# Optimization experiments

Hardware: AMD Instinct MI355X
Metric: run time of the kernel (lower is better)

The kernel has to match this reference:

```python
import jax, jax.numpy as jnp
import numpy as np

B, S, D_IN, D = 2, 192, 1024, 128  # batch, seq_len, input_dim, triaffine_dim


def setup_inputs() -> dict:
    key = jax.random.key(0)
    ks = jax.random.split(key, 10)
    g = lambda k, sh, sc: jax.random.normal(k, sh, jnp.float32) * sc
    return {
        "x": g(ks[0], (B, S, D_IN), 1.0),
        "Wp": g(ks[1], (D_IN, D), 0.02), "bp": jnp.zeros((D,), jnp.float32),
        "Wh": g(ks[2], (D_IN, D), 0.02), "bh": jnp.zeros((D,), jnp.float32),
        "Wt": g(ks[3], (D_IN, D), 0.02), "bt": jnp.zeros((D,), jnp.float32),
        "W_span_ph": g(ks[4], (D, D, D), 0.02),
        "W_span_pt": g(ks[5], (D, D, D), 0.02),
        "W_ph_sib": g(ks[6], (D, D, D), 0.02),
        "W_pt_sib": g(ks[7], (D, D, D), 0.02),
        "W_ph_cop": g(ks[8], (D, D, D), 0.02),
        "W_pt_cop": g(ks[9], (D, D, D), 0.02),
    }


def _mlp(x, W, b):
    # supar-style MLP: Linear + LeakyReLU(0.1); dropout is identity at eval time
    return jax.nn.leaky_relu(x @ W + b, negative_slope=0.1)


def _triaffine(x, y, z, w):
    # supar Triaffine (n_out=1, no bias): s[b,z,x,y] = x_i W_ikj z_k y_j
    wz = jnp.einsum('bzk,ikj->bzij', z, w)          # [b,s,d,d]
    return jnp.einsum('bxi,bzij,byj->bzxy', x, wz, y)  # [b,s,s,s]


def _sym(s):
    # s.triu() + s.triu(1).transpose(-1,-2) over last two dims
    n = s.shape[-1]
    up = jnp.triu(jnp.ones((n, n), bool))
    up1 = jnp.triu(jnp.ones((n, n), bool), 1)
    zero = jnp.zeros((), s.dtype)
    return jnp.where(up, s, zero) + jnp.swapaxes(jnp.where(up1, s, zero), -1, -2)


def reference(x, Wp, bp, Wh, bh, Wt, bt,
              W_span_ph, W_span_pt, W_ph_sib, W_pt_sib, W_ph_cop, W_pt_cop):
    p = _mlp(x, Wp, bp)
    sh = _mlp(x, Wh, bh)   # shared_span: sh_mlp = h_mlp
    st = _mlp(x, Wt, bt)   # shared_span: st_mlp = t_mlp
    span_pst = _sym(_triaffine(sh, st, p, W_span_pt))
    span_psh = _sym(_triaffine(sh, st, p, W_span_ph))
    ph_sib = _sym(_triaffine(sh, sh, p, W_ph_sib))
    pt_sib = _sym(_triaffine(st, st, p, W_pt_sib))
    # co-parent scores: [b,z,x,y] -> permute(0,2,3,1) -> [b,x,y,z]
    ph_cop = jnp.transpose(_triaffine(p, p, sh, W_ph_cop), (0, 2, 3, 1))
    pt_cop = jnp.transpose(_sym(_triaffine(p, p, st, W_pt_cop)), (0, 2, 3, 1))
    return (span_psh, span_pst, ph_sib, pt_sib, ph_cop, pt_cop)
```

## Files before the change

kernel.cpp:

```cpp
#include <hip/hip_runtime.h>

#define SS 192
#define DD 128
#define SAN 16384
#define PITCH 136

typedef short bf8v __attribute__((ext_vector_type(8)));
typedef float f4v  __attribute__((ext_vector_type(4)));

__device__ __forceinline__ unsigned short f2bf(float f) {
    union { float f; unsigned u; } v; v.f = f;
    unsigned r = v.u + 0x7fffu + ((v.u >> 16) & 1u);
    return (unsigned short)(r >> 16);
}

__device__ __forceinline__ f4v mfma16(bf8v a, bf8v b, f4v c) {
    return __builtin_amdgcn_mfma_f32_16x16x32_bf16(a, b, c, 0, 0, 0);
}

__global__ __launch_bounds__(256) void proj_kernel(
    const float* __restrict__ x,
    const float* __restrict__ Wp, const float* __restrict__ bp,
    const float* __restrict__ Wh, const float* __restrict__ bh,
    const float* __restrict__ Wt, const float* __restrict__ bt,
    unsigned short* __restrict__ Pb, unsigned short* __restrict__ SHb,
    unsigned short* __restrict__ STb)
{
    __shared__ float xs[8 * 1024];
    int r0 = blockIdx.x * 8;
    int w  = blockIdx.y;
    const float* W    = (w == 0) ? Wp : (w == 1) ? Wh : Wt;
    const float* bias = (w == 0) ? bp : (w == 1) ? bh : bt;
    unsigned short* O = (w == 0) ? Pb : (w == 1) ? SHb : STb;
    int tid = threadIdx.x;
    for (int u = tid; u < 2048; u += 256)
        *(float4*)(&xs[u * 4]) = *(const float4*)(&x[(size_t)r0 * 1024 + (size_t)u * 4]);
    __syncthreads();
    int col = tid & 127, rg = tid >> 7;
    float acc[4] = {0.f, 0.f, 0.f, 0.f};
    for (int k = 0; k < 1024; ++k) {
        float wv = W[(size_t)k * 128 + col];
        #pragma unroll
        for (int r = 0; r < 4; ++r) acc[r] += xs[(rg * 4 + r) * 1024 + k] * wv;
    }
    float bb = bias[col];
    #pragma unroll
    for (int r = 0; r < 4; ++r) {
        float v = acc[r] + bb;
        v = v > 0.f ? v : 0.1f * v;
        O[(size_t)(r0 + rg * 4 + r) * 128 + col] = f2bf(v);
    }
}

__global__ __launch_bounds__(256) void prep_rev(
    const float* __restrict__ w0, const float* __restrict__ w1,
    const float* __restrict__ w2, const float* __restrict__ w3,
    unsigned short* __restrict__ Wprep)
{
    __shared__ float tile[32][33];
    int sel = blockIdx.z;
    const float* in = (sel == 0) ? w0 : (sel == 1) ? w1 : (sel == 2) ? w2 : w3;
    unsigned short* out = Wprep + (size_t)sel * 2097152;
    int i  = blockIdx.y;
    int kt = (blockIdx.x >> 2) * 32, jt = (blockIdx.x & 3) * 32;
    int tx = threadIdx.x & 31, ty = threadIdx.x >> 5;
    #pragma unroll
    for (int r = 0; r < 4; ++r) {
        int k = kt + ty + r * 8;
        tile[ty + r * 8][tx] = in[((size_t)i * 128 + k) * 128 + jt + tx];
    }
    __syncthreads();
    #pragma unroll
    for (int r = 0; r < 4; ++r) {
        int j = jt + ty + r * 8;
        out[((size_t)j * 128 + i) * 128 + kt + tx] = f2bf(tile[tx][ty + r * 8]);
    }
}

__global__ __launch_bounds__(256) void prep_cop(
    const float* __restrict__ in0, const float* __restrict__ in1,
    unsigned short* __restrict__ Wprep)
{
    __shared__ float tile[32][33];
    int sel = blockIdx.z;
    const float* in = sel ? in1 : in0;
    unsigned short* out = Wprep + (size_t)(4 + sel) * 2097152;
    int k  = blockIdx.y;
    int it = (blockIdx.x >> 2) * 32, jt = (blockIdx.x & 3) * 32;
    int tx = threadIdx.x & 31, ty = threadIdx.x >> 5;
    #pragma unroll
    for (int r = 0; r < 4; ++r) {
        int i = it + ty + r * 8;
        tile[ty + r * 8][tx] = in[((size_t)i * 128 + k) * 128 + jt + tx];
    }
    __syncthreads();
    #pragma unroll
    for (int r = 0; r < 4; ++r) {
        int j = jt + ty + r * 8;
        out[((size_t)j * 128 + k) * 128 + it + tx] = f2bf(tile[tx][ty + r * 8]);
    }
}

__global__ __launch_bounds__(256) void stageA(
    const unsigned short* __restrict__ Pb,
    const unsigned short* __restrict__ Wprep, unsigned short* __restrict__ SAout)
{
    __shared__ unsigned short BL[64 * PITCH];
    int slot = blockIdx.y;
    int n0 = blockIdx.x * 64;
    const unsigned short* Wn = Wprep + (size_t)slot * 2097152 + (size_t)n0 * 128;
    unsigned short* Oo = SAout + (size_t)slot * ((size_t)384 * SAN);
    int tid = threadIdx.x;
    for (int u = tid; u < 1024; u += 256) {
        int e = u * 8; int r = e >> 7; int c = e & 127;
        *(uint4*)(&BL[r * PITCH + c]) = *(const uint4*)(&Wn[e]);
    }
    __syncthreads();
    int wave = tid >> 6, lane = tid & 63, m = lane & 15, quad = lane >> 4;
    const unsigned short* br = &BL[(wave * 16 + m) * PITCH + quad * 8];
    bf8v b0 = *(const bf8v*)(br);
    bf8v b1 = *(const bf8v*)(br + 32);
    bf8v b2 = *(const bf8v*)(br + 64);
    bf8v b3 = *(const bf8v*)(br + 96);
    for (int mt = 0; mt < 24; mt += 2) {
        const unsigned short* ar0 = Pb + (size_t)(mt * 16 + m) * 128 + quad * 8;
        const unsigned short* ar1 = ar0 + 16 * 128;
        f4v acc0 = {0.f, 0.f, 0.f, 0.f}, acc1 = {0.f, 0.f, 0.f, 0.f};
        acc0 = mfma16(*(const bf8v*)(ar0),      b0, acc0);
        acc1 = mfma16(*(const bf8v*)(ar1),      b0, acc1);
        acc0 = mfma16(*(const bf8v*)(ar0 + 32), b1, acc0);
        acc1 = mfma16(*(const bf8v*)(ar1 + 32), b1, acc1);
        acc0 = mfma16(*(const bf8v*)(ar0 + 64), b2, acc0);
        acc1 = mfma16(*(const bf8v*)(ar1 + 64), b2, acc1);
        acc0 = mfma16(*(const bf8v*)(ar0 + 96), b3, acc0);
        acc1 = mfma16(*(const bf8v*)(ar1 + 96), b3, acc1);
        unsigned short* orow0 = Oo + (size_t)(mt * 16) * SAN + n0 + wave * 16;
        unsigned short* orow1 = orow0 + (size_t)16 * SAN;
        #pragma unroll
        for (int r = 0; r < 4; ++r) {
            orow0[(size_t)(quad * 4 + r) * SAN + m] = f2bf(acc0[r]);
            orow1[(size_t)(quad * 4 + r) * SAN + m] = f2bf(acc1[r]);
        }
    }
}

__global__ __launch_bounds__(256) void stageB_all(
    const unsigned short* __restrict__ Pb, const unsigned short* __restrict__ SHb,
    const unsigned short* __restrict__ STb, const unsigned short* __restrict__ SA,
    float* __restrict__ out)
{
    __shared__ unsigned short WZT[128 * PITCH];
    __shared__ unsigned short Tst[64 * PITCH];
    const size_t OUTN = (size_t)2 * SS * SS * SS;

    int t  = blockIdx.y;
    int bz = blockIdx.x;
    int b  = bz / SS;
    int tid = threadIdx.x;

    const unsigned short* src = SA + ((size_t)t * 384 + bz) * SAN;
    for (int u = tid; u < 2048; u += 256) {
        int e = u * 8; int j = e >> 7; int i = e & 127;
        *(uint4*)(&WZT[j * PITCH + i]) = *(const uint4*)(&src[e]);
    }
    __syncthreads();

    int wave = tid >> 6, lane = tid & 63, m = lane & 15, quad = lane >> 4;
    unsigned short* Trow = &Tst[wave * 16 * PITCH];
    const unsigned short* Ta = &Tst[(wave * 16 + m) * PITCH + quad * 8];

    if (t < 4) {
        const unsigned short* X = (t == 3) ? STb : SHb;
        const unsigned short* Y = (t == 2) ? SHb : STb;
        float* O = out + (size_t)t * OUTN + (size_t)bz * SS * SS;

        const int mt_tab[4][3] = {{0,7,9},{1,6,8},{2,5,10},{3,4,11}};
        const unsigned short* Xb = X + (size_t)b * SS * DD;
        const unsigned short* Yb = Y + (size_t)b * SS * DD;

        for (int mi = 0; mi < 3; ++mi) {
            int mt = mt_tab[wave][mi];
            const unsigned short* xr = Xb + (size_t)(mt * 16 + m) * DD + quad * 8;
            bf8v a[4];
            a[0] = *(const bf8v*)(xr);
            a[1] = *(const bf8v*)(xr + 32);
            a[2] = *(const bf8v*)(xr + 64);
            a[3] = *(const bf8v*)(xr + 96);

            for (int nt = 0; nt < 8; nt += 2) {
                f4v acc0 = {0.f,0.f,0.f,0.f}, acc1 = {0.f,0.f,0.f,0.f};
                #pragma unroll
                for (int kk = 0; kk < 4; ++kk) {
                    const unsigned short* bp0 = &WZT[(nt * 16 + m) * PITCH + kk * 32 + quad * 8];
                    const unsigned short* bp1 = &WZT[((nt + 1) * 16 + m) * PITCH + kk * 32 + quad * 8];
                    acc0 = mfma16(a[kk], *(const bf8v*)bp0, acc0);
                    acc1 = mfma16(a[kk], *(const bf8v*)bp1, acc1);
                }
                #pragma unroll
                for (int r = 0; r < 4; ++r) {
                    Trow[(quad * 4 + r) * PITCH + nt * 16 + m]       = f2bf(acc0[r]);
                    Trow[(quad * 4 + r) * PITCH + (nt + 1) * 16 + m] = f2bf(acc1[r]);
                }
            }
            bf8v ta[4];
            ta[0] = *(const bf8v*)(Ta);
            ta[1] = *(const bf8v*)(Ta + 32);
            ta[2] = *(const bf8v*)(Ta + 64);
            ta[3] = *(const bf8v*)(Ta + 96);

            int xs_ = mt * 16, cc = m;
            {
                f4v acc = {0.f,0.f,0.f,0.f};
                #pragma unroll
                for (int kk = 0; kk < 4; ++kk) {
                    bf8v bv = *(const bf8v*)(Yb + (size_t)(mt * 16 + m) * DD + kk * 32 + quad * 8);
                    acc = mfma16(ta[kk], bv, acc);
                }
                #pragma unroll
                for (int r = 0; r < 4; ++r) {
                    int rr = quad * 4 + r;
                    if (rr <= cc) O[(size_t)(xs_ + rr) * SS + xs_ + cc] = acc[r];
                    if (cc > rr)  O[(size_t)(xs_ + cc) * SS + xs_ + rr] = acc[r];
                }
            }
            for (int yt = mt + 1; yt < 12; yt += 2) {
                bool pair = (yt + 1 < 12);
                const unsigned short* yb0 = Yb + (size_t)(yt * 16 + m) * DD + quad * 8;
                f4v acc0 = {0.f,0.f,0.f,0.f}, acc1 = {0.f,0.f,0.f,0.f};
                if (pair) {
                    const unsigned short* yb1 = yb0 + 16 * DD;
                    #pragma unroll
                    for (int kk = 0; kk < 4; ++kk) {
                        bf8v bv0 = *(const bf8v*)(yb0 + kk * 32);
                        bf8v bv1 = *(const bf8v*)(yb1 + kk * 32);
                        acc0 = mfma16(ta[kk], bv0, acc0);
                        acc1 = mfma16(ta[kk], bv1, acc1);
                    }
                } else {
                    #pragma unroll
                    for (int kk = 0; kk < 4; ++kk)
                        acc0 = mfma16(ta[kk], *(const bf8v*)(yb0 + kk * 32), acc0);
                }
                int ys0 = yt * 16;
                #pragma unroll
                for (int r = 0; r < 4; ++r)
                    O[(size_t)(xs_ + quad * 4 + r) * SS + ys0 + cc] = acc0[r];
                *(f4v*)(&O[(size_t)(ys0 + cc) * SS + xs_ + quad * 4]) = acc0;
                if (pair) {
                    int ys1 = ys0 + 16;
                    #pragma unroll
                    for (int r = 0; r < 4; ++r)
                        O[(size_t)(xs_ + quad * 4 + r) * SS + ys1 + cc] = acc1[r];
                    *(f4v*)(&O[(size_t)(ys1 + cc) * SS + xs_ + quad * 4]) = acc1;
                }
            }
        }
    } else {
        const unsigned short* Zsrc = (t == 4) ? SHb : STb;
        int x  = bz - b * SS;
        int xt = x >> 4;
        float* Od = out + (size_t)t * OUTN + (size_t)bz * SS * SS;
        float* Om = out + (size_t)t * OUTN + (size_t)b * SS * SS * SS;

        for (int zi = 0; zi < 3; ++zi) {
            int zt = wave * 3 + zi;
            const unsigned short* sr = Zsrc + (size_t)(b * SS + zt * 16 + m) * DD + quad * 8;
            bf8v a[4];
            a[0] = *(const bf8v*)(sr);
            a[1] = *(const bf8v*)(sr + 32);
            a[2] = *(const bf8v*)(sr + 64);
            a[3] = *(const bf8v*)(sr + 96);
            for (int jt = 0; jt < 8; jt += 2) {
                f4v acc0 = {0.f,0.f,0.f,0.f}, acc1 = {0.f,0.f,0.f,0.f};
                #pragma unroll
                for (int kk = 0; kk < 4; ++kk) {
                    const unsigned short* bp0 = &WZT[(jt * 16 + m) * PITCH + kk * 32 + quad * 8];
                    const unsigned short* bp1 = &WZT[((jt + 1) * 16 + m) * PITCH + kk * 32 + quad * 8];
                    acc0 = mfma16(a[kk], *(const bf8v*)bp0, acc0);
                    acc1 = mfma16(a[kk], *(const bf8v*)bp1, acc1);
                }
                #pragma unroll
                for (int r = 0; r < 4; ++r) {
                    Trow[(quad * 4 + r) * PITCH + jt * 16 + m]       = f2bf(acc0[r]);
                    Trow[(quad * 4 + r) * PITCH + (jt + 1) * 16 + m] = f2bf(acc1[r]);
                }
            }
            bf8v tb[4];
            tb[0] = *(const bf8v*)(Ta);
            tb[1] = *(const bf8v*)(Ta + 32);
            tb[2] = *(const bf8v*)(Ta + 64);
            tb[3] = *(const bf8v*)(Ta + 96);

            const unsigned short* Pbase = Pb + (size_t)b * SS * DD;
            int zc = zt * 16 + m;

            if (t == 4) {
                for (int yt = 0; yt < 12; yt += 2) {
                    const unsigned short* p0 = Pbase + (size_t)(yt * 16 + m) * DD + quad * 8;
                    const unsigned short* p1 = p0 + 16 * DD;
                    f4v acc0 = {0.f,0.f,0.f,0.f}, acc1 = {0.f,0.f,0.f,0.f};
                    #pragma unroll
                    for (int kk = 0; kk < 4; ++kk) {
                        bf8v av0 = *(const bf8v*)(p0 + kk * 32);
                        bf8v av1 = *(const bf8v*)(p1 + kk * 32);
                        acc0 = mfma16(av0, tb[kk], acc0);
                        acc1 = mfma16(av1, tb[kk], acc1);
                    }
                    #pragma unroll
                    for (int r = 0; r < 4; ++r) {
                        Od[(size_t)(yt * 16 + quad * 4 + r) * SS + zc]       = acc0[r];
                        Od[(size_t)((yt + 1) * 16 + quad * 4 + r) * SS + zc] = acc1[r];
                    }
                }
            } else {
                {
                    const unsigned short* p0 = Pbase + (size_t)(xt * 16 + m) * DD + quad * 8;
                    f4v acc = {0.f,0.f,0.f,0.f};
                    #pragma unroll
                    for (int kk = 0; kk < 4; ++kk)
                        acc = mfma16(*(const bf8v*)(p0 + kk * 32), tb[kk], acc);
                    #pragma unroll
                    for (int r = 0; r < 4; ++r) {
                        int y = xt * 16 + quad * 4 + r;
                        if (y >= x) Od[(size_t)y * SS + zc] = acc[r];
                        if (y > x)  Om[(size_t)y * SS * SS + (size_t)x * SS + zc] = acc[r];
                    }
                }
                for (int yt = xt + 1; yt < 12; yt += 2) {
                    bool pair = (yt + 1 < 12);
                    const unsigned short* p0 = Pbase + (size_t)(yt * 16 + m) * DD + quad * 8;
                    f4v acc0 = {0.f,0.f,0.f,0.f}, acc1 = {0.f,0.f,0.f,0.f};
                    if (pair) {
                        const unsigned short* p1 = p0 + 16 * DD;
                        #pragma unroll
                        for (int kk = 0; kk < 4; ++kk) {
                            bf8v av0 = *(const bf8v*)(p0 + kk * 32);
                            bf8v av1 = *(const bf8v*)(p1 + kk * 32);
                            acc0 = mfma16(av0, tb[kk], acc0);
                            acc1 = mfma16(av1, tb[kk], acc1);
                        }
                    } else {
                        #pragma unroll
                        for (int kk = 0; kk < 4; ++kk)
                            acc0 = mfma16(*(const bf8v*)(p0 + kk * 32), tb[kk], acc0);
                    }
                    #pragma unroll
                    for (int r = 0; r < 4; ++r) {
                        int y0 = yt * 16 + quad * 4 + r;
                        Od[(size_t)y0 * SS + zc] = acc0[r];
                        Om[(size_t)y0 * SS * SS + (size_t)x * SS + zc] = acc0[r];
                    }
                    if (pair) {
                        #pragma unroll
                        for (int r = 0; r < 4; ++r) {
                            int y1 = (yt + 1) * 16 + quad * 4 + r;
                            Od[(size_t)y1 * SS + zc] = acc1[r];
                            Om[(size_t)y1 * SS * SS + (size_t)x * SS + zc] = acc1[r];
                        }
                    }
                }
            }
        }
    }
}

extern "C" void kernel_launch(void* const* d_in, const int* in_sizes, int n_in,
                              void* d_out, int out_size, void* d_ws, size_t ws_size,
                              hipStream_t stream)
{
    const float* x   = (const float*)d_in[0];
    const float* Wp  = (const float*)d_in[1];
    const float* bp  = (const float*)d_in[2];
    const float* Wh  = (const float*)d_in[3];
    const float* bh  = (const float*)d_in[4];
    const float* Wt  = (const float*)d_in[5];
    const float* bt  = (const float*)d_in[6];
    const float* W_span_ph = (const float*)d_in[7];
    const float* W_span_pt = (const float*)d_in[8];
    const float* W_ph_sib  = (const float*)d_in[9];
    const float* W_pt_sib  = (const float*)d_in[10];
    const float* W_ph_cop  = (const float*)d_in[11];
    const float* W_pt_cop  = (const float*)d_in[12];

    char* ws = (char*)d_ws;
    unsigned short* Pb    = (unsigned short*)ws;
    unsigned short* SHb   = Pb + 384 * 128;
    unsigned short* STb   = SHb + 384 * 128;
    unsigned short* Wprep = (unsigned short*)(ws + 294912);
    unsigned short* SA    = (unsigned short*)(ws + 294912 + (size_t)6 * 2097152 * 2);

    float* out  = (float*)d_out;

    proj_kernel<<<dim3(48, 3), 256, 0, stream>>>(x, Wp, bp, Wh, bh, Wt, bt, Pb, SHb, STb);
    prep_rev<<<dim3(16, 128, 4), 256, 0, stream>>>(W_span_ph, W_span_pt, W_ph_sib,
                                                   W_pt_sib, Wprep);
    prep_cop<<<dim3(16, 128, 2), 256, 0, stream>>>(W_ph_cop, W_pt_cop, Wprep);
    stageA<<<dim3(256, 6), 256, 0, stream>>>(Pb, Wprep, SA);
    stageB_all<<<dim3(384, 6), 256, 0, stream>>>(Pb, SHb, STb, SA, out);
}
```

Baseline: 640.9 us.

## Split projection over K and reorder stageB loops to reuse Y/P fragments across tiles

The projection GEMM is split into four K-chunks written as fp32 partials to scratch (aliasing SA before it is filled), then reduced with bias and LeakyReLU in a finishing kernel, giving 4x more blocks. In stageB, each wave now computes all three of its intermediate T tiles up front, keeps them in registers, and loops once over y tiles so each Y/P row fragment is loaded once and used for three MFMA chains. A launch bound of 3 waves per SIMD caps register use. The costs are higher register pressure, an extra kernel launch and partial-sum traffic.

```diff
diff --git a/kernel.cpp b/kernel.cpp
--- a/kernel.cpp
+++ b/kernel.cpp
@@ -18,37 +18,63 @@
     return __builtin_amdgcn_mfma_f32_16x16x32_bf16(a, b, c, 0, 0, 0);
 }
 
-__global__ __launch_bounds__(256) void proj_kernel(
+__global__ __launch_bounds__(256) void proj_part(
     const float* __restrict__ x,
-    const float* __restrict__ Wp, const float* __restrict__ bp,
-    const float* __restrict__ Wh, const float* __restrict__ bh,
-    const float* __restrict__ Wt, const float* __restrict__ bt,
+    const float* __restrict__ Wp, const float* __restrict__ Wh,
+    const float* __restrict__ Wt, float* __restrict__ part)
+{
+    __shared__ float xs[8 * 256];
+    int r0 = blockIdx.x * 8;
+    int w  = blockIdx.y;
+    int kc = blockIdx.z;
+    const float* W = (w == 0) ? Wp : (w == 1) ? Wh : Wt;
+    int tid = threadIdx.x;
+    for (int u = tid; u < 512; u += 256) {
+        int row = u >> 6, k4 = u & 63;
+        *(float4*)(&xs[row * 256 + k4 * 4]) =
+            *(const float4*)(&x[(size_t)(r0 + row) * 1024 + kc * 256 + k4 * 4]);
+    }
+    __syncthreads();
+    int col = tid & 127, rg = tid >> 7;
+    float acc[4] = {0.f, 0.f, 0.f, 0.f};
+    const float* Wk = W + (size_t)(kc * 256) * 128 + col;
+    #pragma unroll 8
+    for (int k = 0; k < 256; ++k) {
+        float wv = Wk[(size_t)k * 128];
+        #pragma unroll
+        for (int r = 0; r < 4; ++r) acc[r] += xs[(rg * 4 + r) * 256 + k] * wv;
+    }
+    float* pp = part + (((size_t)w * 4 + kc) * 384) * 128;
+    #pragma unroll
+    for (int r = 0; r < 4; ++r)
+        pp[(size_t)(r0 + rg * 4 + r) * 128 + col] = acc[r];
+}
+
+__global__ __launch_bounds__(256) void proj_fin(
+    const float* __restrict__ part,
+    const float* __restrict__ bp, const float* __restrict__ bh,
+    const float* __restrict__ bt,
     unsigned short* __restrict__ Pb, unsigned short* __restrict__ SHb,
     unsigned short* __restrict__ STb)
 {
-    __shared__ float xs[8 * 1024];
     int r0 = blockIdx.x * 8;
     int w  = blockIdx.y;
-    const float* W    = (w == 0) ? Wp : (w == 1) ? Wh : Wt;
     const float* bias = (w == 0) ? bp : (w == 1) ? bh : bt;
     unsigned short* O = (w == 0) ? Pb : (w == 1) ? SHb : STb;
     int tid = threadIdx.x;
-    for (int u = tid; u < 2048; u += 256)
-        *(float4*)(&xs[u * 4]) = *(const float4*)(&x[(size_t)r0 * 1024 + (size_t)u * 4]);
-    __syncthreads();
     int col = tid & 127, rg = tid >> 7;
-    float acc[4] = {0.f, 0.f, 0.f, 0.f};
-    for (int k = 0; k < 1024; ++k) {
-        float wv = W[(size_t)k * 128 + col];
-        #pragma unroll
-        for (int r = 0; r < 4; ++r) acc[r] += xs[(rg * 4 + r) * 1024 + k] * wv;
-    }
+    const float* pw = part + ((size_t)w * 4) * 384 * 128;
     float bb = bias[col];
     #pragma unroll
     for (int r = 0; r < 4; ++r) {
-        float v = acc[r] + bb;
-        v = v > 0.f ? v : 0.1f * v;
-        O[(size_t)(r0 + rg * 4 + r) * 128 + col] = f2bf(v);
+        int row = r0 + rg * 4 + r;
+        float s = pw[(size_t)row * 128 + col]
+                + pw[(size_t)(384 + row) * 128 + col]
+                + pw[(size_t)(2 * 384 + row) * 128 + col]
+                + pw[(size_t)(3 * 384 + row) * 128 + col];
+        s += bb;
+        s = s > 0.f ? s : 0.1f * s;
+        O[(size_t)row * 128 + col] = f2bf(s);
     }
 }
 
@@ -144,7 +170,7 @@
     }
 }
 
-__global__ __launch_bounds__(256) void stageB_all(
+__global__ __launch_bounds__(256, 3) void stageB_all(
     const unsigned short* __restrict__ Pb, const unsigned short* __restrict__ SHb,
     const unsigned short* __restrict__ STb, const unsigned short* __restrict__ SA,
     float* __restrict__ out)
@@ -173,85 +199,81 @@
         const unsigned short* X = (t == 3) ? STb : SHb;
         const unsigned short* Y = (t == 2) ? SHb : STb;
         float* O = out + (size_t)t * OUTN + (size_t)bz * SS * SS;
-
-        const int mt_tab[4][3] = {{0,7,9},{1,6,8},{2,5,10},{3,4,11}};
         const unsigned short* Xb = X + (size_t)b * SS * DD;
         const unsigned short* Yb = Y + (size_t)b * SS * DD;
 
+        int mts[3];
+        mts[0] = wave;
+        mts[1] = 7 - wave;
+        mts[2] = (wave < 2) ? 9 - wave : 8 + wave;
+
+        bf8v ta[3][4];
+        #pragma unroll
         for (int mi = 0; mi < 3; ++mi) {
-            int mt = mt_tab[wave][mi];
+            int mt = mts[mi];
             const unsigned short* xr = Xb + (size_t)(mt * 16 + m) * DD + quad * 8;
-            bf8v a[4];
-            a[0] = *(const bf8v*)(xr);
-            a[1] = *(const bf8v*)(xr + 32);
-            a[2] = *(const bf8v*)(xr + 64);
-            a[3] = *(const bf8v*)(xr + 96);
-
+            bf8v a0 = *(const bf8v*)(xr);
+            bf8v a1 = *(const bf8v*)(xr + 32);
+            bf8v a2 = *(const bf8v*)(xr + 64);
+            bf8v a3 = *(const bf8v*)(xr + 96);
             for (int nt = 0; nt < 8; nt += 2) {
                 f4v acc0 = {0.f,0.f,0.f,0.f}, acc1 = {0.f,0.f,0.f,0.f};
-                #pragma unroll
-                for (int kk = 0; kk < 4; ++kk) {
-                    const unsigned short* bp0 = &WZT[(nt * 16 + m) * PITCH + kk * 32 + quad * 8];
-                    const unsigned short* bp1 = &WZT[((nt + 1) * 16 + m) * PITCH + kk * 32 + quad * 8];
-                    acc0 = mfma16(a[kk], *(const bf8v*)bp0, acc0);
-                    acc1 = mfma16(a[kk], *(const bf8v*)bp1, acc1);
-                }
+                const unsigned short* w0 = &WZT[(nt * 16 + m) * PITCH + quad * 8];
+                const unsigned short* w1 = &WZT[((nt + 1) * 16 + m) * PITCH + quad * 8];
+                acc0 = mfma16(a0, *(const bf8v*)(w0),      acc0);
+                acc1 = mfma16(a0, *(const bf8v*)(w1),      acc1);
+                acc0 = mfma16(a1, *(const bf8v*)(w0 + 32), acc0);
+                acc1 = mfma16(a1, *(const bf8v*)(w1 + 32), acc1);
+                acc0 = mfma16(a2, *(const bf8v*)(w0 + 64), acc0);
+                acc1 = mfma16(a2, *(const bf8v*)(w1 + 64), acc1);
+                acc0 = mfma16(a3, *(const bf8v*)(w0 + 96), acc0);
+                acc1 = mfma16(a3, *(const bf8v*)(w1 + 96), acc1);
                 #pragma unroll
                 for (int r = 0; r < 4; ++r) {
                     Trow[(quad * 4 + r) * PITCH + nt * 16 + m]       = f2bf(acc0[r]);
                     Trow[(quad * 4 + r) * PITCH + (nt + 1) * 16 + m] = f2bf(acc1[r]);
                 }
             }
-            bf8v ta[4];
-            ta[0] = *(const bf8v*)(Ta);
-            ta[1] = *(const bf8v*)(Ta + 32);
-            ta[2] = *(const bf8v*)(Ta + 64);
-            ta[3] = *(const bf8v*)(Ta + 96);
-
-            int xs_ = mt * 16, cc = m;
-            {
+            ta[mi][0] = *(const bf8v*)(Ta);
+            ta[mi][1] = *(const bf8v*)(Ta + 32);
+            ta[mi][2] = *(const bf8v*)(Ta + 64);
+            ta[mi][3] = *(const bf8v*)(Ta + 96);
+        }
+
+        for (int yt = mts[0]; yt < 12; ++yt) {
+            const unsigned short* yr = Yb + (size_t)(yt * 16 + m) * DD + quad * 8;
+            bf8v yv0 = *(const bf8v*)(yr);
+            bf8v yv1 = *(const bf8v*)(yr + 32);
+            bf8v yv2 = *(const bf8v*)(yr + 64);
+            bf8v yv3 = *(const bf8v*)(yr + 96);
+            f4v accs[3];
+            #pragma unroll
+            for (int mi = 0; mi < 3; ++mi) {
                 f4v acc = {0.f,0.f,0.f,0.f};
-                #pragma unroll
-                for (int kk = 0; kk < 4; ++kk) {
-                    bf8v bv = *(const bf8v*)(Yb + (size_t)(mt * 16 + m) * DD + kk * 32 + quad * 8);
-                    acc = mfma16(ta[kk], bv, acc);
-                }
-                #pragma unroll
-                for (int r = 0; r < 4; ++r) {
-                    int rr = quad * 4 + r;
-                    if (rr <= cc) O[(size_t)(xs_ + rr) * SS + xs_ + cc] = acc[r];
-                    if (cc > rr)  O[(size_t)(xs_ + cc) * SS + xs_ + rr] = acc[r];
-                }
-            }
-            for (int yt = mt + 1; yt < 12; yt += 2) {
-                bool pair = (yt + 1 < 12);
-                const unsigned short* yb0 = Yb + (size_t)(yt * 16 + m) * DD + quad * 8;
-                f4v acc0 = {0.f,0.f,0.f,0.f}, acc1 = {0.f,0.f,0.f,0.f};
-                if (pair) {
-                    const unsigned short* yb1 = yb0 + 16 * DD;
+                acc = mfma16(ta[mi][0], yv0, acc);
+                acc = mfma16(ta[mi][1], yv1, acc);
+                acc = mfma16(ta[mi][2], yv2, acc);
+                acc = mfma16(ta[mi][3], yv3, acc);
+                accs[mi] = acc;
+            }
+            #pragma unroll
+            for (int mi = 0; mi < 3; ++mi) {
+                int mt = mts[mi];
+                if (mt > yt) continue;
+                f4v acc = accs[mi];
+                int xs_ = mt * 16, ys_ = yt * 16, cc = m;
+                if (mt == yt) {
                     #pragma unroll
-                    for (int kk = 0; kk < 4; ++kk) {
-                        bf8v bv0 = *(const bf8v*)(yb0 + kk * 32);
-                        bf8v bv1 = *(const bf8v*)(yb1 + kk * 32);
-                        acc0 = mfma16(ta[kk], bv0, acc0);
-                        acc1 = mfma16(ta[kk], bv1, acc1);
+                    for (int r = 0; r < 4; ++r) {
+                        int rr = quad * 4 + r;
+                        if (rr <= cc) O[(size_t)(xs_ + rr) * SS + xs_ + cc] = acc[r];
+                        if (cc > rr)  O[(size_t)(xs_ + cc) * SS + xs_ + rr] = acc[r];
                     }
                 } else {
                     #pragma unroll
-                    for (int kk = 0; kk < 4; ++kk)
-                        acc0 = mfma16(ta[kk], *(const bf8v*)(yb0 + kk * 32), acc0);
-                }
-                int ys0 = yt * 16;
-                #pragma unroll
-                for (int r = 0; r < 4; ++r)
-                    O[(size_t)(xs_ + quad * 4 + r) * SS + ys0 + cc] = acc0[r];
-                *(f4v*)(&O[(size_t)(ys0 + cc) * SS + xs_ + quad * 4]) = acc0;
-                if (pair) {
-                    int ys1 = ys0 + 16;
-                    #pragma unroll
                     for (int r = 0; r < 4; ++r)
-                        O[(size_t)(xs_ + quad * 4 + r) * SS + ys1 + cc] = acc1[r];
-                    *(f4v*)(&O[(size_t)(ys1 + cc) * SS + xs_ + quad * 4]) = acc1;
+                        O[(size_t)(xs_ + quad * 4 + r) * SS + ys_ + cc] = acc[r];
+                    *(f4v*)(&O[(size_t)(ys_ + cc) * SS + xs_ + quad * 4]) = acc;
                 }
             }
         }
@@ -262,101 +284,85 @@
         float* Od = out + (size_t)t * OUTN + (size_t)bz * SS * SS;
         float* Om = out + (size_t)t * OUTN + (size_t)b * SS * SS * SS;
 
+        bf8v tb[3][4];
+        #pragma unroll
         for (int zi = 0; zi < 3; ++zi) {
             int zt = wave * 3 + zi;
             const unsigned short* sr = Zsrc + (size_t)(b * SS + zt * 16 + m) * DD + quad * 8;
-            bf8v a[4];
-            a[0] = *(const bf8v*)(sr);
-            a[1] = *(const bf8v*)(sr + 32);
-            a[2] = *(const bf8v*)(sr + 64);
-            a[3] = *(const bf8v*)(sr + 96);
+            bf8v a0 = *(const bf8v*)(sr);
+            bf8v a1 = *(const bf8v*)(sr + 32);
+            bf8v a2 = *(const bf8v*)(sr + 64);
+            bf8v a3 = *(const bf8v*)(sr + 96);
             for (int jt = 0; jt < 8; jt += 2) {
                 f4v acc0 = {0.f,0.f,0.f,0.f}, acc1 = {0.f,0.f,0.f,0.f};
-                #pragma unroll
-                for (int kk = 0; kk < 4; ++kk) {
-                    const unsigned short* bp0 = &WZT[(jt * 16 + m) * PITCH + kk * 32 + quad * 8];
-                    const unsigned short* bp1 = &WZT[((jt + 1) * 16 + m) * PITCH + kk * 32 + quad * 8];
-                    acc0 = mfma16(a[kk], *(const bf8v*)bp0, acc0);
-                    acc1 = mfma16(a[kk], *(const bf8v*)bp1, acc1);
-                }
+                const unsigned short* w0 = &WZT[(jt * 16 + m) * PITCH + quad * 8];
+                const unsigned short* w1 = &WZT[((jt + 1) * 16 + m) * PITCH + quad * 8];
+                acc0 = mfma16(a0, *(const bf8v*)(w0),      acc0);
+                acc1 = mfma16(a0, *(const bf8v*)(w1),      acc1);
+                acc0 = mfma16(a1, *(const bf8v*)(w0 + 32), acc0);
+                acc1 = mfma16(a1, *(const bf8v*)(w1 + 32), acc1);
+                acc0 = mfma16(a2, *(const bf8v*)(w0 + 64), acc0);
+                acc1 = mfma16(a2, *(const bf8v*)(w1 + 64), acc1);
+                acc0 = mfma16(a3, *(const bf8v*)(w0 + 96), acc0);
+                acc1 = mfma16(a3, *(const bf8v*)(w1 + 96), acc1);
                 #pragma unroll
                 for (int r = 0; r < 4; ++r) {
                     Trow[(quad * 4 + r) * PITCH + jt * 16 + m]       = f2bf(acc0[r]);
                     Trow[(quad * 4 + r) * PITCH + (jt + 1) * 16 + m] = f2bf(acc1[r]);
                 }
             }
-            bf8v tb[4];
-            tb[0] = *(const bf8v*)(Ta);
-            tb[1] = *(const bf8v*)(Ta + 32);
-            tb[2] = *(const bf8v*)(Ta + 64);
-            tb[3] = *(const bf8v*)(Ta + 96);
-
-            const unsigned short* Pbase = Pb + (size_t)b * SS * DD;
-            int zc = zt * 16 + m;
-
+            tb[zi][0] = *(const bf8v*)(Ta);
+            tb[zi][1] = *(const bf8v*)(Ta + 32);
+            tb[zi][2] = *(const bf8v*)(Ta + 64);
+            tb[zi][3] = *(const bf8v*)(Ta + 96);
+        }
+
+        const unsigned short* Pbase = Pb + (size_t)b * SS * DD;
+        int yt0 = (t == 4) ? 0 : xt;
+        for (int yt = yt0; yt < 12; ++yt) {
+            const unsigned short* pr = Pbase + (size_t)(yt * 16 + m) * DD + quad * 8;
+            bf8v pv0 = *(const bf8v*)(pr);
+            bf8v pv1 = *(const bf8v*)(pr + 32);
+            bf8v pv2 = *(const bf8v*)(pr + 64);
+            bf8v pv3 = *(const bf8v*)(pr + 96);
+            f4v accs[3];
+            #pragma unroll
+            for (int zi = 0; zi < 3; ++zi) {
+                f4v acc = {0.f,0.f,0.f,0.f};
+                acc = mfma16(pv0, tb[zi][0], acc);
+                acc = mfma16(pv1, tb[zi][1], acc);
+                acc = mfma16(pv2, tb[zi][2], acc);
+                acc = mfma16(pv3, tb[zi][3], acc);
+                accs[zi] = acc;
+            }
             if (t == 4) {
-                for (int yt = 0; yt < 12; yt += 2) {
-                    const unsigned short* p0 = Pbase + (size_t)(yt * 16 + m) * DD + quad * 8;
-                    const unsigned short* p1 = p0 + 16 * DD;
-                    f4v acc0 = {0.f,0.f,0.f,0.f}, acc1 = {0.f,0.f,0.f,0.f};
+                #pragma unroll
+                for (int zi = 0; zi < 3; ++zi) {
+                    int zc = (wave * 3 + zi) * 16 + m;
                     #pragma unroll
-                    for (int kk = 0; kk < 4; ++kk) {
-                        bf8v av0 = *(const bf8v*)(p0 + kk * 32);
-                        bf8v av1 = *(const bf8v*)(p1 + kk * 32);
-                        acc0 = mfma16(av0, tb[kk], acc0);
-                        acc1 = mfma16(av1, tb[kk], acc1);
-                    }
+                    for (int r = 0; r < 4; ++r)
+                        Od[(size_t)(yt * 16 + quad * 4 + r) * SS + zc] = accs[zi][r];
+                }
+            } else if (yt == xt) {
+                #pragma unroll
+                for (int zi = 0; zi < 3; ++zi) {
+                    int zc = (wave * 3 + zi) * 16 + m;
                     #pragma unroll
                     for (int r = 0; r < 4; ++r) {
-                        Od[(size_t)(yt * 16 + quad * 4 + r) * SS + zc]       = acc0[r];
-                        Od[(size_t)((yt + 1) * 16 + quad * 4 + r) * SS + zc] = acc1[r];
+                        int y = yt * 16 + quad * 4 + r;
+                        if (y >= x) Od[(size_t)y * SS + zc] = accs[zi][r];
+                        if (y > x)  Om[(size_t)y * SS * SS + (size_t)x * SS + zc] = accs[zi][r];
                     }
                 }
             } else {
-                {
-                    const unsigned short* p0 = Pbase + (size_t)(xt * 16 + m) * DD + quad * 8;
-                    f4v acc = {0.f,0.f,0.f,0.f};
-                    #pragma unroll
-                    for (int kk = 0; kk < 4; ++kk)
-                        acc = mfma16(*(const bf8v*)(p0 + kk * 32), tb[kk], acc);
+                #pragma unroll
+                for (int zi = 0; zi < 3; ++zi) {
+                    int zc = (wave * 3 + zi) * 16 + m;
                     #pragma unroll
                     for (int r = 0; r < 4; ++r) {
-                        int y = xt * 16 + quad * 4 + r;
-                        if (y >= x) Od[(size_t)y * SS + zc] = acc[r];
-                        if (y > x)  Om[(size_t)y * SS * SS + (size_t)x * SS + zc] = acc[r];
-                    }
-                }
-                for (int yt = xt + 1; yt < 12; yt += 2) {
-                    bool pair = (yt + 1 < 12);
-                    const unsigned short* p0 = Pbase + (size_t)(yt * 16 + m) * DD + quad * 8;
-                    f4v acc0 = {0.f,0.f,0.f,0.f}, acc1 = {0.f,0.f,0.f,0.f};
-                    if (pair) {
-                        const unsigned short* p1 = p0 + 16 * DD;
-                        #pragma unroll
-                        for (int kk = 0; kk < 4; ++kk) {
-                            bf8v av0 = *(const bf8v*)(p0 + kk * 32);
-                            bf8v av1 = *(const bf8v*)(p1 + kk * 32);
-                            acc0 = mfma16(av0, tb[kk], acc0);
-                            acc1 = mfma16(av1, tb[kk], acc1);
-                        }
-                    } else {
-                        #pragma unroll
-                        for (int kk = 0; kk < 4; ++kk)
-                            acc0 = mfma16(*(const bf8v*)(p0 + kk * 32), tb[kk], acc0);
-                    }
-                    #pragma unroll
-                    for (int r = 0; r < 4; ++r) {
-                        int y0 = yt * 16 + quad * 4 + r;
-                        Od[(size_t)y0 * SS + zc] = acc0[r];
-                        Om[(size_t)y0 * SS * SS + (size_t)x * SS + zc] = acc0[r];
-                    }
-                    if (pair) {
-                        #pragma unroll
-                        for (int r = 0; r < 4; ++r) {
-                            int y1 = (yt + 1) * 16 + quad * 4 + r;
-                            Od[(size_t)y1 * SS + zc] = acc1[r];
-                            Om[(size_t)y1 * SS * SS + (size_t)x * SS + zc] = acc1[r];
-                        }
+                        int y = yt * 16 + quad * 4 + r;
+                        Od[(size_t)y * SS + zc] = accs[zi][r];
+                        Om[(size_t)y * SS * SS + (size_t)x * SS + zc] = accs[zi][r];
                     }
                 }
             }
@@ -388,10 +394,12 @@
     unsigned short* STb   = SHb + 384 * 128;
     unsigned short* Wprep = (unsigned short*)(ws + 294912);
     unsigned short* SA    = (unsigned short*)(ws + 294912 + (size_t)6 * 2097152 * 2);
+    float* part = (float*)SA;
 
     float* out  = (float*)d_out;
 
-    proj_kernel<<<dim3(48, 3), 256, 0, stream>>>(x, Wp, bp, Wh, bh, Wt, bt, Pb, SHb, STb);
+    proj_part<<<dim3(48, 3, 4), 256, 0, stream>>>(x, Wp, Wh, Wt, part);
+    proj_fin<<<dim3(48, 3), 256, 0, stream>>>(part, bp, bh, bt, Pb, SHb, STb);
     prep_rev<<<dim3(16, 128, 4), 256, 0, stream>>>(W_span_ph, W_span_pt, W_ph_sib,
                                                    W_pt_sib, Wprep);
     prep_cop<<<dim3(16, 128, 2), 256, 0, stream>>>(W_ph_cop, W_pt_cop, Wprep);
```

Result: faster. 563.6 us (-12.1%).
